# Performance work log

Hardware: AMD Instinct MI355X
Metric: run time of the kernel (lower is better)

## Reference

```python
import jax, jax.numpy as jnp
import numpy as np

N, E, D = 50000, 1600000, 3     # nodes, edges, pseudo-coordinate dim
IN_F, OUT_F = 32, 32
KS = 4                           # kernel size per dim (open spline)
K = KS ** D                      # 64 kernel weight matrices
S = 2 ** D                       # (degree+1)^D basis combos for degree-1 splines


def setup_inputs() -> dict:
    key = jax.random.key(0)
    k1, k2, k3, k4, k5 = jax.random.split(key, 5)
    features = jax.random.normal(k1, (N, IN_F), jnp.float32)
    pseudo = jax.random.uniform(k2, (E, D), jnp.float32)      # normalized edge attrs in [0,1]
    stdv = 1.0 / np.sqrt(IN_F * K)
    weight = jax.random.uniform(k3, (K, IN_F, OUT_F), jnp.float32, -stdv, stdv)
    bias = jax.random.uniform(k4, (OUT_F,), jnp.float32, -stdv, stdv)
    edge_index = jax.random.randint(k5, (2, E), 0, N, jnp.int32)
    return {"features": features, "pseudo": pseudo, "weight": weight,
            "bias": bias, "edge_index": edge_index}


def _spline_basis(pseudo):
    """Degree-1 open B-spline basis. Returns (w [S,E], flat_idx [S,E])."""
    v = pseudo * (KS - 1)                                   # open-spline scaling
    bot = jnp.clip(jnp.floor(v), 0, KS - 2).astype(jnp.int32)   # [E,D]
    frac = v - bot.astype(v.dtype)                          # [E,D] in [0,1]
    bits = (jnp.arange(S)[:, None] >> jnp.arange(D)[None, :]) & 1   # [S,D]
    idx = bot[None, :, :] + bits[:, None, :]                # [S,E,D] in [0,KS-1]
    w = jnp.where(bits[:, None, :] == 1, frac[None], 1.0 - frac[None]).prod(-1)  # [S,E]
    strides = (KS ** jnp.arange(D)).astype(jnp.int32)
    flat = (idx * strides).sum(-1)                          # [S,E] in [0,K-1]
    return w, flat


def reference(features, pseudo, weight, bias, edge_index):
    row, col = edge_index[0], edge_index[1]                 # target, source
    w, flat = _spline_basis(pseudo)
    # Pre-transform features by every kernel weight matrix: [N,K,OUT]
    Z = jnp.einsum('ni,kio->nko', features, weight)
    # Per-edge message: sum over the S active basis functions (irregular gather)
    msg = jnp.zeros((E, OUT_F), Z.dtype)
    for s in range(S):                                      # S=8, fixed small loop
        msg = msg + w[s][:, None] * Z[col, flat[s]]
    # Scatter-mean to target nodes
    out = jax.ops.segment_sum(msg, row, num_segments=N)
    deg = jax.ops.segment_sum(jnp.ones((E,), features.dtype), row, num_segments=N)
    return out / jnp.maximum(deg, 1.0)[:, None] + bias
```

## Files before the change

### kernel.cpp

```cpp
#include <hip/hip_runtime.h>
#include <hip/hip_bf16.h>

#define NN 50000
#define EE 1600000
#define BPB 96
#define CH 1024
#define NCHUNK ((EE + CH - 1) / CH)
#define GG 128
#define GSZ (EE / GG)

typedef __attribute__((ext_vector_type(8))) short    s16x8;
typedef __attribute__((ext_vector_type(4))) float    f32x4;
typedef __attribute__((ext_vector_type(2))) unsigned u32x2;
typedef __attribute__((ext_vector_type(4))) unsigned u32x4;

static __device__ __forceinline__ short f2bs(float x) {
  __hip_bfloat16 h = __float2bfloat16(x);
  short s; __builtin_memcpy(&s, &h, 2); return s;
}

__constant__ int kOffs[8] = {0, 1, 4, 5, 16, 17, 20, 21};

__global__ __launch_bounds__(256) void group_rank(const int* __restrict__ ei,
                                                  unsigned short* __restrict__ lrank,
                                                  int* __restrict__ gcnt) {
  __shared__ unsigned lh32[NN / 2];
  for (int j = threadIdx.x; j < NN / 2; j += 256) lh32[j] = 0;
  __syncthreads();
  const int g  = blockIdx.x;
  const int e0 = g * GSZ;
  for (int i = threadIdx.x; i < GSZ; i += 256) {
    int e = e0 + i;
    int row = ei[e];
    unsigned add = (row & 1) ? 0x10000u : 1u;
    unsigned ret = atomicAdd(&lh32[row >> 1], add);
    unsigned r = (row & 1) ? (ret >> 16) : (ret & 0xFFFFu);
    lrank[e] = (unsigned short)r;
  }
  __syncthreads();
  for (int j = threadIdx.x; j < NN / 2; j += 256) {
    unsigned u = lh32[j];
    gcnt[(size_t)g * NN + 2 * j]     = (int)(u & 0xFFFFu);
    gcnt[(size_t)g * NN + 2 * j + 1] = (int)(u >> 16);
  }
}

#define PREP_BLOCKS (160 + NCHUNK)
__global__ __launch_bounds__(256) void prep(const float* __restrict__ W,
                                            const float* __restrict__ f,
                                            const float* __restrict__ pseudo,
                                            short* __restrict__ Wb,
                                            short* __restrict__ fbh,
                                            int* __restrict__ bh) {
  const int b = blockIdx.x;
  if (b < 32) {
    int tid = b * 256 + threadIdx.x;
    int t = tid >> 6, l = tid & 63;
    int c = t * 16 + (l & 15);
    int k0 = (l >> 4) * 8;
    s16x8 frag;
#pragma unroll
    for (int j = 0; j < 8; ++j)
      frag[j] = f2bs(W[(c >> 5) * 1024 + (k0 + j) * 32 + (c & 31)]);
    ((s16x8*)Wb)[tid] = frag;
  } else if (b < 160) {
    for (int tid = (b - 32) * 256 + threadIdx.x; tid < NN * 32 / 8; tid += 128 * 256) {
      const f32x4* fp = (const f32x4*)f + (size_t)tid * 2;
      f32x4 a = fp[0], c = fp[1];
      s16x8 o;
#pragma unroll
      for (int j = 0; j < 4; ++j) { o[j] = f2bs(a[j]); o[4 + j] = f2bs(c[j]); }
      ((s16x8*)fbh)[tid] = o;
    }
  } else {
    __shared__ int lh[27];
    if (threadIdx.x < 27) lh[threadIdx.x] = 0;
    __syncthreads();
    const int c  = b - 160;
    const int e0 = c * CH;
#pragma unroll
    for (int i = 0; i < CH / 256; ++i) {
      int e = e0 + i * 256 + threadIdx.x;
      if (e < EE) {
        float v0 = pseudo[e * 3 + 0] * 3.0f;
        float v1 = pseudo[e * 3 + 1] * 3.0f;
        float v2 = pseudo[e * 3 + 2] * 3.0f;
        int b0 = (int)fminf(fmaxf(floorf(v0), 0.0f), 2.0f);
        int b1 = (int)fminf(fmaxf(floorf(v1), 0.0f), 2.0f);
        int b2 = (int)fminf(fmaxf(floorf(v2), 0.0f), 2.0f);
        atomicAdd(&lh[b0 + 3 * b1 + 9 * b2], 1);
      }
    }
    __syncthreads();
    if (threadIdx.x < 27) bh[threadIdx.x * NCHUNK + c] = lh[threadIdx.x];
  }
}

__global__ __launch_bounds__(256) void deg_total(const int* __restrict__ gcnt,
                                                 int* __restrict__ degi) {
  int row = blockIdx.x * 256 + threadIdx.x;
  if (row >= NN) return;
  int s = 0;
#pragma unroll 8
  for (int g = 0; g < GG; ++g) s += gcnt[(size_t)g * NN + row];
  degi[row] = s;
}

__global__ __launch_bounds__(1024) void scan_combo(int* __restrict__ bh,
                                                   const int* __restrict__ degi,
                                                   int* __restrict__ bstart,
                                                   int* __restrict__ rstart) {
  __shared__ int carry;
  __shared__ int tot;
  __shared__ int wsum[16];
  const int lane = threadIdx.x & 63;
  const int wid  = threadIdx.x >> 6;
  if (threadIdx.x == 0) carry = 0;
  __syncthreads();
  if (blockIdx.x == 0) {
    const int L = 27 * NCHUNK;
    for (int c0 = 0; c0 < L; c0 += 1024) {
      int i = c0 + threadIdx.x;
      int v = (i < L) ? bh[i] : 0;
      int x = v;
#pragma unroll
      for (int d = 1; d < 64; d <<= 1) {
        int y = __shfl_up(x, d, 64);
        if (lane >= d) x += y;
      }
      if (lane == 63) wsum[wid] = x;
      __syncthreads();
      if (threadIdx.x == 0) {
        int run = 0;
#pragma unroll
        for (int w = 0; w < 16; ++w) { int t = wsum[w]; wsum[w] = run; run += t; }
        tot = run;
      }
      __syncthreads();
      int excl = carry + wsum[wid] + (x - v);
      if (i < L) bh[i] = excl;
      __syncthreads();
      if (threadIdx.x == 0) carry += tot;
      __syncthreads();
    }
    if (threadIdx.x < 27) bstart[threadIdx.x] = bh[threadIdx.x * NCHUNK];
    if (threadIdx.x == 27) bstart[27] = EE;
  } else {
    for (int c0 = 0; c0 < NN; c0 += 1024) {
      int i = c0 + threadIdx.x;
      int v = (i < NN) ? degi[i] : 0;
      int x = v;
#pragma unroll
      for (int d = 1; d < 64; d <<= 1) {
        int y = __shfl_up(x, d, 64);
        if (lane >= d) x += y;
      }
      if (lane == 63) wsum[wid] = x;
      __syncthreads();
      if (threadIdx.x == 0) {
        int run = 0;
#pragma unroll
        for (int w = 0; w < 16; ++w) { int t = wsum[w]; wsum[w] = run; run += t; }
        tot = run;
      }
      __syncthreads();
      int excl = carry + wsum[wid] + (x - v);
      if (i < NN) rstart[i] = excl;
      __syncthreads();
      if (threadIdx.x == 0) carry += tot;
      __syncthreads();
    }
    if (threadIdx.x == 0) rstart[NN] = carry;
  }
}

__global__ __launch_bounds__(256) void group_base(int* __restrict__ gcnt,
                                                  const int* __restrict__ rstart) {
  int row = blockIdx.x * 256 + threadIdx.x;
  if (row >= NN) return;
  int run = rstart[row];
  for (int g0 = 0; g0 < GG; g0 += 8) {
    int t[8];
#pragma unroll
    for (int j = 0; j < 8; ++j) t[j] = gcnt[(size_t)(g0 + j) * NN + row];
#pragma unroll
    for (int j = 0; j < 8; ++j) {
      int v = t[j];
      gcnt[(size_t)(g0 + j) * NN + row] = run;
      run += v;
    }
  }
}

static __device__ __forceinline__ unsigned q16(float fr) {
  return min((unsigned)(fr * 65536.0f), 65535u);
}
__global__ __launch_bounds__(256) void bucket_scatter(const float* __restrict__ pseudo,
                                                      const int* __restrict__ ei,
                                                      const unsigned short* __restrict__ lrank,
                                                      const int* __restrict__ gcnt,
                                                      const int* __restrict__ bh,
                                                      u32x2* __restrict__ edata,
                                                      int* __restrict__ rpos_arr) {
  __shared__ int lh[27];
  __shared__ int bb[27];
  if (threadIdx.x < 27) {
    lh[threadIdx.x] = 0;
    bb[threadIdx.x] = bh[threadIdx.x * NCHUNK + blockIdx.x];
  }
  __syncthreads();
  const int e0 = blockIdx.x * CH;
#pragma unroll
  for (int i = 0; i < CH / 256; ++i) {
    int e = e0 + i * 256 + threadIdx.x;
    if (e < EE) {
      float v0 = pseudo[e * 3 + 0] * 3.0f;
      float v1 = pseudo[e * 3 + 1] * 3.0f;
      float v2 = pseudo[e * 3 + 2] * 3.0f;
      float fb0 = fmaxf(fminf(floorf(v0), 2.0f), 0.0f);
      float fb1 = fmaxf(fminf(floorf(v1), 2.0f), 0.0f);
      float fb2 = fmaxf(fminf(floorf(v2), 2.0f), 0.0f);
      int q = (int)fb0 + 3 * (int)fb1 + 9 * (int)fb2;
      int rk = atomicAdd(&lh[q], 1);
      int pos = bb[q] + rk;
      int row = ei[e];
      int col = ei[EE + e];
      int ge  = e / GSZ;
      u32x2 pk;
      pk.x = q16(v0 - fb0) | (q16(v1 - fb1) << 16);
      pk.y = q16(v2 - fb2) | ((unsigned)col << 16);
      edata[pos] = pk;
      rpos_arr[pos] = gcnt[(size_t)ge * NN + row] + (int)lrank[e];
    }
  }
}

__global__ __launch_bounds__(256) void edge_mfma_nw(const u32x2* __restrict__ edata,
                                                    const int* __restrict__ rpos_arr,
                                                    const short* __restrict__ fbh,
                                                    const short* __restrict__ Wb,
                                                    const int* __restrict__ bstart,
                                                    u32x4* __restrict__ msg4) {
  const int q   = blockIdx.x / BPB;
  const int sub = blockIdx.x % BPB;
  const int l   = threadIdx.x & 63;
  const int wid = threadIdx.x >> 6;

  const int start = bstart[q];
  const int end   = bstart[q + 1];
  const int nE    = end - start;
  if (nE <= 0) return;
  const int ngroups = (nE + 15) >> 4;

  const int b0 = q % 3, b1 = (q / 3) % 3, b2 = q / 9;
  const int base = b0 + 4 * b1 + 16 * b2;
  const int ko[8] = {0, 1, 4, 5, 16, 17, 20, 21};

  s16x8 bf[8][2];
#pragma unroll
  for (int s = 0; s < 8; ++s) {
    int kmat = base + ko[s];
#pragma unroll
    for (int oh = 0; oh < 2; ++oh)
      bf[s][oh] = ((const s16x8*)Wb)[(kmat * 2 + oh) * 64 + l];
  }

  const int m   = l & 15;
  const int kq  = l >> 4;
  const int stride = BPB * 4;
  const float inv16 = 1.0f / 65536.0f;

  int gA = sub * 4 + wid;
  if (gA >= ngroups) return;
  int gB = gA + stride;

  int iA = start + gA * 16 + m;  int ciA = iA < end ? iA : start;
  int iB = start + gB * 16 + m;  int ciB = (gB < ngroups && iB < end) ? iB : start;

  u32x2 edA = edata[ciA];  int rpA = rpos_arr[ciA];
  u32x2 edB = edata[ciB];  int rpB = rpos_arr[ciB];
  s16x8 afA = ((const s16x8*)fbh)[(size_t)(edA.y >> 16) * 4 + kq];

  while (true) {
    const bool moreB = gB < ngroups;
    const int gC = gB + stride;
    int iC = start + gC * 16 + m;
    int ciC = (gC < ngroups && iC < end) ? iC : start;
    u32x2 edC = edata[ciC];
    int   rpC = rpos_arr[ciC];
    s16x8 afB = ((const s16x8*)fbh)[(size_t)(edB.y >> 16) * 4 + kq];

    float f0 = (float)(edA.x & 0xFFFFu) * inv16;
    float f1 = (float)(edA.x >> 16)     * inv16;
    float f2 = (float)(edA.y & 0xFFFFu) * inv16;
    float g0 = 1.0f - f0, g1c = 1.0f - f1, g2c = 1.0f - f2;
    float w8[8];
    w8[0] = g0 * g1c * g2c; w8[1] = f0 * g1c * g2c;
    w8[2] = g0 * f1 * g2c;  w8[3] = f0 * f1 * g2c;
    w8[4] = g0 * g1c * f2;  w8[5] = f0 * g1c * f2;
    w8[6] = g0 * f1 * f2;   w8[7] = f0 * f1 * f2;

    f32x4 acc0 = {0.f, 0.f, 0.f, 0.f}, acc1 = {0.f, 0.f, 0.f, 0.f};
#pragma unroll
    for (int s = 0; s < 8; ++s) {
      f32x4 d0 = __builtin_amdgcn_mfma_f32_16x16x32_bf16(bf[s][0], afA,
                   (f32x4){0.f, 0.f, 0.f, 0.f}, 0, 0, 0);
      f32x4 d1 = __builtin_amdgcn_mfma_f32_16x16x32_bf16(bf[s][1], afA,
                   (f32x4){0.f, 0.f, 0.f, 0.f}, 0, 0, 0);
      float ws = w8[s];
#pragma unroll
      for (int r = 0; r < 4; ++r) {
        acc0[r] += ws * d0[r];
        acc1[r] += ws * d1[r];
      }
    }

    if (gA * 16 + m < nE) {
      u32x4 pk;
      pk.x = (unsigned)(unsigned short)f2bs(acc0[0]) |
             ((unsigned)(unsigned short)f2bs(acc1[0]) << 16);
      pk.y = (unsigned)(unsigned short)f2bs(acc0[1]) |
             ((unsigned)(unsigned short)f2bs(acc1[1]) << 16);
      pk.z = (unsigned)(unsigned short)f2bs(acc0[2]) |
             ((unsigned)(unsigned short)f2bs(acc1[2]) << 16);
      pk.w = (unsigned)(unsigned short)f2bs(acc0[3]) |
             ((unsigned)(unsigned short)f2bs(acc1[3]) << 16);
      msg4[(size_t)rpA * 4 + kq] = pk;
    }

    if (!moreB) break;
    gA = gB; edA = edB; rpA = rpB; afA = afB;
    gB = gC; edB = edC; rpB = rpC;
  }
}

__global__ __launch_bounds__(256) void gather_out(const unsigned* __restrict__ msg,
                                                  const int* __restrict__ rstart,
                                                  const float* __restrict__ bias,
                                                  float* __restrict__ out) {
  int n = (blockIdx.x * 256 + threadIdx.x) >> 4;
  int j = threadIdx.x & 15;
  if (n >= NN) return;
  int s = rstart[n], e = rstart[n + 1];
  int cnt = e - s;
  const unsigned* mp = msg + (size_t)s * 16 + j;
  float s0 = 0.f, s1 = 0.f;
  int i = 0;
  for (; i + 4 <= cnt; i += 4) {
    unsigned uA = mp[(size_t)(i + 0) * 16];
    unsigned uB = mp[(size_t)(i + 1) * 16];
    unsigned uC = mp[(size_t)(i + 2) * 16];
    unsigned uD = mp[(size_t)(i + 3) * 16];
    s0 += __uint_as_float(uA << 16); s1 += __uint_as_float(uA & 0xFFFF0000u);
    s0 += __uint_as_float(uB << 16); s1 += __uint_as_float(uB & 0xFFFF0000u);
    s0 += __uint_as_float(uC << 16); s1 += __uint_as_float(uC & 0xFFFF0000u);
    s0 += __uint_as_float(uD << 16); s1 += __uint_as_float(uD & 0xFFFF0000u);
  }
  for (; i < cnt; ++i) {
    unsigned u = mp[(size_t)i * 16];
    s0 += __uint_as_float(u << 16);
    s1 += __uint_as_float(u & 0xFFFF0000u);
  }
  float d = fmaxf((float)cnt, 1.0f);
  out[n * 32 + j]      = s0 / d + bias[j];
  out[n * 32 + 16 + j] = s1 / d + bias[16 + j];
}

static __device__ __forceinline__ void spline_basis(const float* __restrict__ pseudo,
                                                    int e, float w[8], int& base) {
  float v0 = pseudo[e * 3 + 0] * 3.0f;
  float v1 = pseudo[e * 3 + 1] * 3.0f;
  float v2 = pseudo[e * 3 + 2] * 3.0f;
  float b0 = fmaxf(fminf(floorf(v0), 2.0f), 0.0f);
  float b1 = fmaxf(fminf(floorf(v1), 2.0f), 0.0f);
  float b2 = fmaxf(fminf(floorf(v2), 2.0f), 0.0f);
  float f0 = v0 - b0, f1 = v1 - b1, f2 = v2 - b2;
  float g0 = 1.0f - f0, g1 = 1.0f - f1, g2 = 1.0f - f2;
  base = (int)b0 + 4 * (int)b1 + 16 * (int)b2;
  w[0] = g0 * g1 * g2; w[1] = f0 * g1 * g2;
  w[2] = g0 * f1 * g2; w[3] = f0 * f1 * g2;
  w[4] = g0 * g1 * f2; w[5] = f0 * g1 * f2;
  w[6] = g0 * f1 * f2; w[7] = f0 * f1 * f2;
}

__global__ __launch_bounds__(256) void edge_direct(const float* __restrict__ pseudo,
                                                   const int* __restrict__ ei,
                                                   const float* __restrict__ f,
                                                   const float* __restrict__ W,
                                                   float* __restrict__ acc,
                                                   float* __restrict__ deg) {
  const int tid = blockIdx.x * 256 + threadIdx.x;
  const int e = tid >> 5;
  const int o = tid & 31;
  if (e >= EE) return;
  const int row = ei[e];
  const int col = ei[EE + e];
  float w[8]; int base;
  spline_basis(pseudo, e, w, base);
  const float myf = f[col * 32 + o];
  float a = 0.0f;
  for (int i = 0; i < 32; ++i) {
    float fi = __shfl(myf, i, 32);
    float wsum = 0.0f;
#pragma unroll
    for (int s = 0; s < 8; ++s)
      wsum += w[s] * W[(size_t)(base + kOffs[s]) * 1024 + i * 32 + o];
    a += fi * wsum;
  }
  atomicAdd(acc + (size_t)row * 32 + o, a);
  if (o == 0) atomicAdd(deg + row, 1.0f);
}

__global__ __launch_bounds__(256) void finalize(const float* __restrict__ acc,
                                                const float* __restrict__ deg,
                                                const float* __restrict__ bias,
                                                float* __restrict__ out) {
  int tid = blockIdx.x * 256 + threadIdx.x;
  if (tid >= NN * 32) return;
  int n = tid >> 5, o = tid & 31;
  float d = fmaxf(deg[n], 1.0f);
  out[tid] = acc[tid] / d + bias[o];
}

extern "C" void kernel_launch(void* const* d_in, const int* in_sizes, int n_in,
                              void* d_out, int out_size, void* d_ws, size_t ws_size,
                              hipStream_t stream) {
  const float* f      = (const float*)d_in[0];
  const float* pseudo = (const float*)d_in[1];
  const float* W      = (const float*)d_in[2];
  const float* bias   = (const float*)d_in[3];
  const int*   ei     = (const int*)d_in[4];
  float* out = (float*)d_out;

  constexpr size_t DEGI_OFF  = 0;
  constexpr size_t BST_OFF   = 200064;
  constexpr size_t RST_OFF   = 200192;
  constexpr size_t BH_OFF    = 400256;
  constexpr size_t LRANK_OFF = 569088;
  constexpr size_t GCNT_OFF  = LRANK_OFF + (size_t)EE * 2;
  constexpr size_t ED_OFF    = GCNT_OFF + (size_t)GG * NN * 4;
  constexpr size_t RPOS_OFF  = ED_OFF + (size_t)EE * 8;
  constexpr size_t MSG_OFF   = RPOS_OFF + (size_t)EE * 4;
  constexpr size_t FBH_OFF   = MSG_OFF + (size_t)EE * 64;
  constexpr size_t WB_OFF    = FBH_OFF + (size_t)NN * 64;
  constexpr size_t TOTAL     = WB_OFF + 128 * 64 * 8 * 2;

  char* ws = (char*)d_ws;

  if (ws_size >= TOTAL) {
    int*            degi  = (int*)(ws + DEGI_OFF);
    int*            bst   = (int*)(ws + BST_OFF);
    int*            rst   = (int*)(ws + RST_OFF);
    int*            bh    = (int*)(ws + BH_OFF);
    unsigned short* lrank = (unsigned short*)(ws + LRANK_OFF);
    int*            gcnt  = (int*)(ws + GCNT_OFF);
    u32x2*          edata = (u32x2*)(ws + ED_OFF);
    int*            rpos  = (int*)(ws + RPOS_OFF);
    u32x4*          msg4  = (u32x4*)(ws + MSG_OFF);
    unsigned*       msg   = (unsigned*)(ws + MSG_OFF);
    short*          fbh   = (short*)(ws + FBH_OFF);
    short*          Wb    = (short*)(ws + WB_OFF);

    group_rank<<<GG, 256, 0, stream>>>(ei, lrank, gcnt);
    prep<<<PREP_BLOCKS, 256, 0, stream>>>(W, f, pseudo, Wb, fbh, bh);
    deg_total<<<(NN + 255) / 256, 256, 0, stream>>>(gcnt, degi);
    scan_combo<<<2, 1024, 0, stream>>>(bh, degi, bst, rst);
    group_base<<<(NN + 255) / 256, 256, 0, stream>>>(gcnt, rst);
    bucket_scatter<<<NCHUNK, 256, 0, stream>>>(pseudo, ei, lrank, gcnt, bh, edata, rpos);
    edge_mfma_nw<<<27 * BPB, 256, 0, stream>>>(edata, rpos, fbh, Wb, bst, msg4);
    gather_out<<<(NN * 16 + 255) / 256, 256, 0, stream>>>(msg, rst, bias, out);
  } else {
    constexpr size_t ACC_SZ = (size_t)NN * 32 * 4;
    float* acc = (float*)ws;
    float* deg = (float*)(ws + ACC_SZ);
    hipMemsetAsync(acc, 0, ACC_SZ + (size_t)NN * 4, stream);
    edge_direct<<<(EE * 32) / 256, 256, 0, stream>>>(pseudo, ei, f, W, acc, deg);
    finalize<<<(NN * 32) / 256, 256, 0, stream>>>(acc, deg, bias, out);
  }
}
```

Baseline: 277.8 us.

## Replace single-block serial scans with a three-phase multi-block reduce-then-scan

The two-block serial scan over node degrees and bucket histograms is replaced by a parallel three-phase scheme. The first kernel fuses degree totals with per-block partial sums, a tiny kernel scans those partials, and a third kernel applies the offsets across many blocks. This removes a long serial chain that ran on only two workgroups, at the cost of one more kernel launch and extra small workspace buffers.

```diff
diff --git a/kernel.cpp b/kernel.cpp
--- a/kernel.cpp
+++ b/kernel.cpp
@@ -8,6 +8,7 @@
 #define NCHUNK ((EE + CH - 1) / CH)
 #define GG 128
 #define GSZ (EE / GG)
+#define NRB 196
 
 typedef __attribute__((ext_vector_type(8))) short    s16x8;
 typedef __attribute__((ext_vector_type(4))) float    f32x4;
@@ -96,32 +97,102 @@
   }
 }
 
-__global__ __launch_bounds__(256) void deg_total(const int* __restrict__ gcnt,
-                                                 int* __restrict__ degi) {
-  int row = blockIdx.x * 256 + threadIdx.x;
-  if (row >= NN) return;
-  int s = 0;
-#pragma unroll 8
-  for (int g = 0; g < GG; ++g) s += gcnt[(size_t)g * NN + row];
-  degi[row] = s;
-}
-
-__global__ __launch_bounds__(1024) void scan_combo(int* __restrict__ bh,
-                                                   const int* __restrict__ degi,
-                                                   int* __restrict__ bstart,
-                                                   int* __restrict__ rstart) {
-  __shared__ int carry;
-  __shared__ int tot;
-  __shared__ int wsum[16];
+__global__ __launch_bounds__(256) void sum_p1(const int* __restrict__ gcnt,
+                                              const int* __restrict__ bh,
+                                              int* __restrict__ degi,
+                                              int* __restrict__ rpart,
+                                              int* __restrict__ btot) {
+  const int b = blockIdx.x;
   const int lane = threadIdx.x & 63;
   const int wid  = threadIdx.x >> 6;
-  if (threadIdx.x == 0) carry = 0;
+  __shared__ int ws[4];
+  if (b < NRB) {
+    int row = b * 256 + threadIdx.x;
+    int s = 0;
+    if (row < NN) {
+#pragma unroll 8
+      for (int g = 0; g < GG; ++g) s += gcnt[(size_t)g * NN + row];
+      degi[row] = s;
+    }
+    int x = s;
+#pragma unroll
+    for (int d = 1; d < 64; d <<= 1) x += __shfl_xor(x, d, 64);
+    if (lane == 0) ws[wid] = x;
+    __syncthreads();
+    if (threadIdx.x == 0) rpart[b] = ws[0] + ws[1] + ws[2] + ws[3];
+  } else {
+    int q = b - NRB;
+    if (q >= 27) return;
+    int s = 0;
+    for (int c = threadIdx.x; c < NCHUNK; c += 256) s += bh[q * NCHUNK + c];
+    int x = s;
+#pragma unroll
+    for (int d = 1; d < 64; d <<= 1) x += __shfl_xor(x, d, 64);
+    if (lane == 0) ws[wid] = x;
+    __syncthreads();
+    if (threadIdx.x == 0) btot[q] = ws[0] + ws[1] + ws[2] + ws[3];
+  }
+}
+
+__global__ __launch_bounds__(256) void scan_tiny(const int* __restrict__ rpart,
+                                                 const int* __restrict__ btot,
+                                                 int* __restrict__ rpartx,
+                                                 int* __restrict__ bstart) {
+  __shared__ int sA[256];
+  __shared__ int sB[32];
+  const int t = threadIdx.x;
+  int origA = (t < NRB) ? rpart[t] : 0;
+  sA[t] = origA;
+  int origB = 0;
+  if (t < 32) { origB = (t < 27) ? btot[t] : 0; sB[t] = origB; }
   __syncthreads();
-  if (blockIdx.x == 0) {
-    const int L = 27 * NCHUNK;
-    for (int c0 = 0; c0 < L; c0 += 1024) {
-      int i = c0 + threadIdx.x;
-      int v = (i < L) ? bh[i] : 0;
+#pragma unroll
+  for (int d = 1; d < 256; d <<= 1) {
+    int a = (t >= d) ? sA[t - d] : 0;
+    int bb = (t < 32 && d < 32 && t >= d) ? sB[t - d] : 0;
+    __syncthreads();
+    sA[t] += a;
+    if (t < 32 && d < 32) sB[t] += bb;
+    __syncthreads();
+  }
+  if (t < NRB) rpartx[t] = sA[t] - origA;
+  if (t < 27)  bstart[t] = sB[t] - origB;
+  if (t == 27) bstart[27] = EE;
+}
+
+__global__ __launch_bounds__(256) void scan_p3(int* __restrict__ bh,
+                                               const int* __restrict__ degi,
+                                               const int* __restrict__ rpartx,
+                                               const int* __restrict__ bstart,
+                                               int* __restrict__ rstart) {
+  const int b = blockIdx.x;
+  const int lane = threadIdx.x & 63;
+  const int wid  = threadIdx.x >> 6;
+  __shared__ int wsum[4];
+  __shared__ int ctot;
+  if (b < NRB) {
+    int row = b * 256 + threadIdx.x;
+    int v = (row < NN) ? degi[row] : 0;
+    int x = v;
+#pragma unroll
+    for (int d = 1; d < 64; d <<= 1) {
+      int y = __shfl_up(x, d, 64);
+      if (lane >= d) x += y;
+    }
+    if (lane == 63) wsum[wid] = x;
+    __syncthreads();
+    int off = 0;
+#pragma unroll
+    for (int w = 0; w < 4; ++w) if (w < wid) off += wsum[w];
+    if (row < NN) rstart[row] = rpartx[b] + off + (x - v);
+    if (b == 0 && threadIdx.x == 0) rstart[NN] = EE;
+  } else {
+    int q = b - NRB;
+    if (q >= 27) return;
+    int carry = bstart[q];
+    for (int c0 = 0; c0 < NCHUNK; c0 += 256) {
+      int c = c0 + threadIdx.x;
+      int v = (c < NCHUNK) ? bh[q * NCHUNK + c] : 0;
       int x = v;
 #pragma unroll
       for (int d = 1; d < 64; d <<= 1) {
@@ -130,47 +201,15 @@
       }
       if (lane == 63) wsum[wid] = x;
       __syncthreads();
-      if (threadIdx.x == 0) {
-        int run = 0;
-#pragma unroll
-        for (int w = 0; w < 16; ++w) { int t = wsum[w]; wsum[w] = run; run += t; }
-        tot = run;
-      }
+      int off = 0;
+#pragma unroll
+      for (int w = 0; w < 4; ++w) if (w < wid) off += wsum[w];
+      if (c < NCHUNK) bh[q * NCHUNK + c] = carry + off + (x - v);
       __syncthreads();
-      int excl = carry + wsum[wid] + (x - v);
-      if (i < L) bh[i] = excl;
+      if (threadIdx.x == 0) ctot = wsum[0] + wsum[1] + wsum[2] + wsum[3];
       __syncthreads();
-      if (threadIdx.x == 0) carry += tot;
-      __syncthreads();
-    }
-    if (threadIdx.x < 27) bstart[threadIdx.x] = bh[threadIdx.x * NCHUNK];
-    if (threadIdx.x == 27) bstart[27] = EE;
-  } else {
-    for (int c0 = 0; c0 < NN; c0 += 1024) {
-      int i = c0 + threadIdx.x;
-      int v = (i < NN) ? degi[i] : 0;
-      int x = v;
-#pragma unroll
-      for (int d = 1; d < 64; d <<= 1) {
-        int y = __shfl_up(x, d, 64);
-        if (lane >= d) x += y;
-      }
-      if (lane == 63) wsum[wid] = x;
-      __syncthreads();
-      if (threadIdx.x == 0) {
-        int run = 0;
-#pragma unroll
-        for (int w = 0; w < 16; ++w) { int t = wsum[w]; wsum[w] = run; run += t; }
-        tot = run;
-      }
-      __syncthreads();
-      int excl = carry + wsum[wid] + (x - v);
-      if (i < NN) rstart[i] = excl;
-      __syncthreads();
-      if (threadIdx.x == 0) carry += tot;
-      __syncthreads();
-    }
-    if (threadIdx.x == 0) rstart[NN] = carry;
+      carry += ctot;
+    }
   }
 }
 
@@ -432,39 +471,46 @@
   const int*   ei     = (const int*)d_in[4];
   float* out = (float*)d_out;
 
-  constexpr size_t DEGI_OFF  = 0;
-  constexpr size_t BST_OFF   = 200064;
-  constexpr size_t RST_OFF   = 200192;
-  constexpr size_t BH_OFF    = 400256;
-  constexpr size_t LRANK_OFF = 569088;
-  constexpr size_t GCNT_OFF  = LRANK_OFF + (size_t)EE * 2;
-  constexpr size_t ED_OFF    = GCNT_OFF + (size_t)GG * NN * 4;
-  constexpr size_t RPOS_OFF  = ED_OFF + (size_t)EE * 8;
-  constexpr size_t MSG_OFF   = RPOS_OFF + (size_t)EE * 4;
-  constexpr size_t FBH_OFF   = MSG_OFF + (size_t)EE * 64;
-  constexpr size_t WB_OFF    = FBH_OFF + (size_t)NN * 64;
-  constexpr size_t TOTAL     = WB_OFF + 128 * 64 * 8 * 2;
+  constexpr size_t DEGI_OFF   = 0;
+  constexpr size_t RPART_OFF  = 200064;
+  constexpr size_t BTOT_OFF   = 200960;
+  constexpr size_t RPARTX_OFF = 201088;
+  constexpr size_t BST_OFF    = 201984;
+  constexpr size_t RST_OFF    = 202112;
+  constexpr size_t BH_OFF     = 402176;
+  constexpr size_t LRANK_OFF  = 571008;
+  constexpr size_t GCNT_OFF   = LRANK_OFF + (size_t)EE * 2;
+  constexpr size_t ED_OFF     = GCNT_OFF + (size_t)GG * NN * 4;
+  constexpr size_t RPOS_OFF   = ED_OFF + (size_t)EE * 8;
+  constexpr size_t MSG_OFF    = RPOS_OFF + (size_t)EE * 4;
+  constexpr size_t FBH_OFF    = MSG_OFF + (size_t)EE * 64;
+  constexpr size_t WB_OFF     = FBH_OFF + (size_t)NN * 64;
+  constexpr size_t TOTAL      = WB_OFF + 128 * 64 * 8 * 2;
 
   char* ws = (char*)d_ws;
 
   if (ws_size >= TOTAL) {
-    int*            degi  = (int*)(ws + DEGI_OFF);
-    int*            bst   = (int*)(ws + BST_OFF);
-    int*            rst   = (int*)(ws + RST_OFF);
-    int*            bh    = (int*)(ws + BH_OFF);
-    unsigned short* lrank = (unsigned short*)(ws + LRANK_OFF);
-    int*            gcnt  = (int*)(ws + GCNT_OFF);
-    u32x2*          edata = (u32x2*)(ws + ED_OFF);
-    int*            rpos  = (int*)(ws + RPOS_OFF);
-    u32x4*          msg4  = (u32x4*)(ws + MSG_OFF);
-    unsigned*       msg   = (unsigned*)(ws + MSG_OFF);
-    short*          fbh   = (short*)(ws + FBH_OFF);
-    short*          Wb    = (short*)(ws + WB_OFF);
+    int*            degi   = (int*)(ws + DEGI_OFF);
+    int*            rpart  = (int*)(ws + RPART_OFF);
+    int*            btot   = (int*)(ws + BTOT_OFF);
+    int*            rpartx = (int*)(ws + RPARTX_OFF);
+    int*            bst    = (int*)(ws + BST_OFF);
+    int*            rst    = (int*)(ws + RST_OFF);
+    int*            bh     = (int*)(ws + BH_OFF);
+    unsigned short* lrank  = (unsigned short*)(ws + LRANK_OFF);
+    int*            gcnt   = (int*)(ws + GCNT_OFF);
+    u32x2*          edata  = (u32x2*)(ws + ED_OFF);
+    int*            rpos   = (int*)(ws + RPOS_OFF);
+    u32x4*          msg4   = (u32x4*)(ws + MSG_OFF);
+    unsigned*       msg    = (unsigned*)(ws + MSG_OFF);
+    short*          fbh    = (short*)(ws + FBH_OFF);
+    short*          Wb     = (short*)(ws + WB_OFF);
 
     group_rank<<<GG, 256, 0, stream>>>(ei, lrank, gcnt);
     prep<<<PREP_BLOCKS, 256, 0, stream>>>(W, f, pseudo, Wb, fbh, bh);
-    deg_total<<<(NN + 255) / 256, 256, 0, stream>>>(gcnt, degi);
-    scan_combo<<<2, 1024, 0, stream>>>(bh, degi, bst, rst);
+    sum_p1<<<NRB + 27, 256, 0, stream>>>(gcnt, bh, degi, rpart, btot);
+    scan_tiny<<<1, 256, 0, stream>>>(rpart, btot, rpartx, bst);
+    scan_p3<<<NRB + 27, 256, 0, stream>>>(bh, degi, rpartx, bst, rst);
     group_base<<<(NN + 255) / 256, 256, 0, stream>>>(gcnt, rst);
     bucket_scatter<<<NCHUNK, 256, 0, stream>>>(pseudo, ei, lrank, gcnt, bh, edata, rpos);
     edge_mfma_nw<<<27 * BPB, 256, 0, stream>>>(edata, rpos, fbh, Wb, bst, msg4);
```

Result: faster. 252.4 us (-9.2%).
